# Kernel optimization log

Hardware: AMD Instinct MI355X
Metric: run time of the kernel (lower is better)

The kernel has to match this reference:

```python
import jax, jax.numpy as jnp
import numpy as np

N = 4096
D = 512
H = 3


def setup_inputs() -> dict:
    key = jax.random.key(0)
    k1, k2, k3 = jax.random.split(key, 3)
    graph_info = (jax.random.uniform(k1, (N, N)) < 0.01).astype(jnp.float32)
    h = jax.random.normal(k2, (N, D), dtype=jnp.float32)
    # xavier_normal_ with relu gain: std = sqrt(2) * sqrt(2/(fan_in+fan_out))
    std = np.sqrt(2.0) * np.sqrt(2.0 / (D + H))
    P = jax.random.normal(k3, (D, H), dtype=jnp.float32) * jnp.float32(std)
    return {"graph_info": graph_info, "h": h, "P": P}


def reference(graph_info, h, P):
    # graph_info_1 = spmm(graph_info^T, I)^T == graph_info (identity densification)
    mask = graph_info > 0                                  # [N, N]
    E = jax.nn.relu(h @ P)                                 # [N, H] per-node scores, all heads
    NEG = jnp.float32(-9e15)
    # e is broadcast along rows: att[i, j] = E[j, k] where edge (i->j) exists
    logits = jnp.where(mask[None, :, :], E.T[:, None, :], NEG)  # [H, N, N]
    att = jax.nn.softmax(logits, axis=-1)                  # row-softmax per head
    hh = jnp.einsum('hij,jd->hid', att, h)                 # [H, N, D] aggregate
    # sum_flag == 1: scale each row i by its degree (rowsum of graph_info_1)
    rowsum = jnp.sum(graph_info, axis=-1)                  # [N]
    hh = hh * rowsum[None, :, None]
    # multi_head > 1, concat=False: sum over heads
    return jnp.sum(hh, axis=0)                             # [N, D]
```

## Files before the change

### kernel.cpp

```cpp
#include <hip/hip_runtime.h>
#include <stdint.h>

#define NN 4096
#define DD 512
#define NH 3
#define MAXDEG 256

__device__ __forceinline__ unsigned short f2bf_rn(float x) {
    union { float f; uint32_t u; } v; v.f = x;
    uint32_t u = v.u;
    uint32_t r = (u + 0x7FFFu + ((u >> 16) & 1u)) >> 16;
    return (unsigned short)r;
}
__device__ __forceinline__ float bflo(uint32_t u) {
    union { uint32_t u; float f; } v; v.u = u << 16; return v.f;
}
__device__ __forceinline__ float bfhi(uint32_t u) {
    union { uint32_t u; float f; } v; v.u = u & 0xFFFF0000u; return v.f;
}

__global__ __launch_bounds__(256) void prep_kernel(
    const float* __restrict__ h, const float* __restrict__ P,
    float* __restrict__ w, unsigned short* __restrict__ hb)
{
    int gid = blockIdx.x * 256 + threadIdx.x;
    int row = gid >> 6, ln = gid & 63;
    const float4* h4 = (const float4*)(h + (size_t)row * DD);
    float4 va = h4[ln * 2], vb = h4[ln * 2 + 1];
    float e[8] = { va.x, va.y, va.z, va.w, vb.x, vb.y, vb.z, vb.w };

    uint32_t pk0 = (uint32_t)f2bf_rn(e[0]) | ((uint32_t)f2bf_rn(e[1]) << 16);
    uint32_t pk1 = (uint32_t)f2bf_rn(e[2]) | ((uint32_t)f2bf_rn(e[3]) << 16);
    uint32_t pk2 = (uint32_t)f2bf_rn(e[4]) | ((uint32_t)f2bf_rn(e[5]) << 16);
    uint32_t pk3 = (uint32_t)f2bf_rn(e[6]) | ((uint32_t)f2bf_rn(e[7]) << 16);
    uint4 pk = make_uint4(pk0, pk1, pk2, pk3);
    *(uint4*)(hb + (size_t)row * DD + ln * 8) = pk;

    int d0 = ln * 8;
    float a0 = 0.f, a1 = 0.f, a2 = 0.f;
    #pragma unroll
    for (int k = 0; k < 8; ++k) {
        float hv = e[k];
        const float* Pr = P + (size_t)(d0 + k) * NH;
        a0 = fmaf(hv, Pr[0], a0);
        a1 = fmaf(hv, Pr[1], a1);
        a2 = fmaf(hv, Pr[2], a2);
    }
    #pragma unroll
    for (int off = 32; off > 0; off >>= 1) {
        a0 += __shfl_down(a0, off);
        a1 += __shfl_down(a1, off);
        a2 += __shfl_down(a2, off);
    }
    if (ln == 0) {
        w[row * NH + 0] = expf(fmaxf(a0, 0.f));
        w[row * NH + 1] = expf(fmaxf(a1, 0.f));
        w[row * NH + 2] = expf(fmaxf(a2, 0.f));
    }
}

__global__ __launch_bounds__(256) void att_agg_kernel(
    const float* __restrict__ g, const unsigned short* __restrict__ hb,
    const float* __restrict__ w, float* __restrict__ out)
{
    __shared__ int   s_idx[MAXDEG + 4];
    __shared__ float s_c[MAXDEG + 4];
    __shared__ int   s_cnt;
    __shared__ float s_z[4][3];
    __shared__ float s_part[4][DD];

    const int row = blockIdx.x, tid = threadIdx.x;
    const int wv = tid >> 6, ln = tid & 63;
    if (tid == 0) s_cnt = 0;
    __syncthreads();

    const float4* g4 = (const float4*)(g + (size_t)row * NN);
    #pragma unroll
    for (int it = 0; it < (NN / 4) / 256; ++it) {
        int c4 = it * 256 + tid;
        float4 v = g4[c4];
        float comp[4] = { v.x, v.y, v.z, v.w };
        int base = c4 * 4;
        #pragma unroll
        for (int k = 0; k < 4; ++k) {
            bool p = comp[k] > 0.f;
            unsigned long long m = __ballot(p);
            if (m) {
                int nset = __popcll(m);
                int bpos;
                if (ln == 0) bpos = atomicAdd(&s_cnt, nset);
                bpos = __shfl(bpos, 0);
                if (p) {
                    unsigned pre = __builtin_amdgcn_mbcnt_lo((unsigned)m, 0u);
                    pre = __builtin_amdgcn_mbcnt_hi((unsigned)(m >> 32), pre);
                    int pos = bpos + (int)pre;
                    if (pos < MAXDEG) s_idx[pos] = base + k;
                }
            }
        }
    }
    __syncthreads();
    int nnz = s_cnt; if (nnz > MAXDEG) nnz = MAXDEG;

    if (nnz == 0) {
        ((float2*)(out + (size_t)row * DD))[tid] = make_float2(0.f, 0.f);
        return;
    }

    float z0 = 0.f, z1 = 0.f, z2 = 0.f, w0 = 0.f, w1 = 0.f, w2 = 0.f;
    int myj = 0;
    if (tid < nnz) {
        myj = s_idx[tid];
        const float* wr = w + (size_t)myj * NH;
        w0 = wr[0]; w1 = wr[1]; w2 = wr[2];
        z0 = w0; z1 = w1; z2 = w2;
    }
    #pragma unroll
    for (int off = 32; off > 0; off >>= 1) {
        z0 += __shfl_down(z0, off);
        z1 += __shfl_down(z1, off);
        z2 += __shfl_down(z2, off);
    }
    if (ln == 0) { s_z[wv][0] = z0; s_z[wv][1] = z1; s_z[wv][2] = z2; }
    __syncthreads();
    float Z0 = s_z[0][0] + s_z[1][0] + s_z[2][0] + s_z[3][0];
    float Z1 = s_z[0][1] + s_z[1][1] + s_z[2][1] + s_z[3][1];
    float Z2 = s_z[0][2] + s_z[1][2] + s_z[2][2] + s_z[3][2];
    float RS = (float)nnz;
    float sc0 = RS / Z0, sc1 = RS / Z1, sc2 = RS / Z2;

    int npad = (nnz + 3) & ~3;
    if (tid < nnz) s_c[tid] = fmaf(sc0, w0, fmaf(sc1, w1, sc2 * w2));
    else if (tid < npad) { s_idx[tid] = 0; s_c[tid] = 0.f; }
    __syncthreads();

    int nq = npad >> 2;
    float acc0=0.f,acc1=0.f,acc2=0.f,acc3=0.f,acc4=0.f,acc5=0.f,acc6=0.f,acc7=0.f;
    const unsigned short* hcol = hb + ln * 8;
    int q = 0;
    for (; q + 1 < nq; q += 2) {
        int t0 = q * 4 + wv, t1 = t0 + 4;
        int ja = s_idx[t0]; float ca = s_c[t0];
        int jb = s_idx[t1]; float cb = s_c[t1];
        uint4 ra = *(const uint4*)(hcol + (size_t)ja * DD);
        uint4 rb = *(const uint4*)(hcol + (size_t)jb * DD);
        acc0 = fmaf(ca, bflo(ra.x), acc0); acc1 = fmaf(ca, bfhi(ra.x), acc1);
        acc2 = fmaf(ca, bflo(ra.y), acc2); acc3 = fmaf(ca, bfhi(ra.y), acc3);
        acc4 = fmaf(ca, bflo(ra.z), acc4); acc5 = fmaf(ca, bfhi(ra.z), acc5);
        acc6 = fmaf(ca, bflo(ra.w), acc6); acc7 = fmaf(ca, bfhi(ra.w), acc7);
        acc0 = fmaf(cb, bflo(rb.x), acc0); acc1 = fmaf(cb, bfhi(rb.x), acc1);
        acc2 = fmaf(cb, bflo(rb.y), acc2); acc3 = fmaf(cb, bfhi(rb.y), acc3);
        acc4 = fmaf(cb, bflo(rb.z), acc4); acc5 = fmaf(cb, bfhi(rb.z), acc5);
        acc6 = fmaf(cb, bflo(rb.w), acc6); acc7 = fmaf(cb, bfhi(rb.w), acc7);
    }
    if (q < nq) {
        int t0 = q * 4 + wv;
        int ja = s_idx[t0]; float ca = s_c[t0];
        uint4 ra = *(const uint4*)(hcol + (size_t)ja * DD);
        acc0 = fmaf(ca, bflo(ra.x), acc0); acc1 = fmaf(ca, bfhi(ra.x), acc1);
        acc2 = fmaf(ca, bflo(ra.y), acc2); acc3 = fmaf(ca, bfhi(ra.y), acc3);
        acc4 = fmaf(ca, bflo(ra.z), acc4); acc5 = fmaf(ca, bfhi(ra.z), acc5);
        acc6 = fmaf(ca, bflo(ra.w), acc6); acc7 = fmaf(ca, bfhi(ra.w), acc7);
    }

    float4* sp = (float4*)&s_part[wv][ln * 8];
    sp[0] = make_float4(acc0, acc1, acc2, acc3);
    sp[1] = make_float4(acc4, acc5, acc6, acc7);
    __syncthreads();
    int c0 = tid * 2;
    float2 p0 = *(const float2*)&s_part[0][c0];
    float2 p1 = *(const float2*)&s_part[1][c0];
    float2 p2 = *(const float2*)&s_part[2][c0];
    float2 p3 = *(const float2*)&s_part[3][c0];
    float r0 = (p0.x + p1.x) + (p2.x + p3.x);
    float r1 = (p0.y + p1.y) + (p2.y + p3.y);
    ((float2*)(out + (size_t)row * DD))[tid] = make_float2(r0, r1);
}

extern "C" void kernel_launch(void* const* d_in, const int* in_sizes, int n_in,
                              void* d_out, int out_size, void* d_ws, size_t ws_size,
                              hipStream_t stream) {
    const float* g = (const float*)d_in[0];
    const float* h = (const float*)d_in[1];
    const float* P = (const float*)d_in[2];
    float* out = (float*)d_out;

    float* w = (float*)d_ws;
    unsigned short* hb = (unsigned short*)((char*)d_ws + 65536);

    prep_kernel<<<(NN * 64) / 256, 256, 0, stream>>>(h, P, w, hb);
    att_agg_kernel<<<NN, 256, 0, stream>>>(g, hb, w, out);
}
```

Before: 113.1 us.

## Process one row per wavefront and drop block-level synchronization

Each wavefront now handles a whole row: it scans the adjacency row, compacts neighbor indices into its own shared buffer, computes the softmax normalizers and gathers bf16 features alone. This removes shared atomics, __syncthreads and the cross-wave partial-sum reduction through shared memory, and launches a quarter as many blocks. Nontemporal loads and stores are used for the streamed adjacency, h and output. The trade-off is fewer waves per row, so each wave does a longer serial gather over all neighbors with less latency hiding per row.

```diff
diff --git a/kernel.cpp b/kernel.cpp
--- a/kernel.cpp
+++ b/kernel.cpp
@@ -5,6 +5,8 @@
 #define DD 512
 #define NH 3
 #define MAXDEG 256
+
+typedef float f4v __attribute__((ext_vector_type(4)));
 
 __device__ __forceinline__ unsigned short f2bf_rn(float x) {
     union { float f; uint32_t u; } v; v.f = x;
@@ -25,9 +27,10 @@
 {
     int gid = blockIdx.x * 256 + threadIdx.x;
     int row = gid >> 6, ln = gid & 63;
-    const float4* h4 = (const float4*)(h + (size_t)row * DD);
-    float4 va = h4[ln * 2], vb = h4[ln * 2 + 1];
-    float e[8] = { va.x, va.y, va.z, va.w, vb.x, vb.y, vb.z, vb.w };
+    const f4v* h4 = (const f4v*)(h + (size_t)row * DD);
+    f4v va = __builtin_nontemporal_load(&h4[ln * 2]);
+    f4v vb = __builtin_nontemporal_load(&h4[ln * 2 + 1]);
+    float e[8] = { va[0], va[1], va[2], va[3], vb[0], vb[1], vb[2], vb[3] };
 
     uint32_t pk0 = (uint32_t)f2bf_rn(e[0]) | ((uint32_t)f2bf_rn(e[1]) << 16);
     uint32_t pk1 = (uint32_t)f2bf_rn(e[2]) | ((uint32_t)f2bf_rn(e[3]) << 16);
@@ -63,118 +66,108 @@
     const float* __restrict__ g, const unsigned short* __restrict__ hb,
     const float* __restrict__ w, float* __restrict__ out)
 {
-    __shared__ int   s_idx[MAXDEG + 4];
-    __shared__ float s_c[MAXDEG + 4];
-    __shared__ int   s_cnt;
-    __shared__ float s_z[4][3];
-    __shared__ float s_part[4][DD];
+    __shared__ int   s_idx[4][MAXDEG + 8];
+    __shared__ float s_c[4][MAXDEG + 8];
 
-    const int row = blockIdx.x, tid = threadIdx.x;
-    const int wv = tid >> 6, ln = tid & 63;
-    if (tid == 0) s_cnt = 0;
-    __syncthreads();
+    const int wv = threadIdx.x >> 6, ln = threadIdx.x & 63;
+    const int row = blockIdx.x * 4 + wv;
+    int*   __restrict__ idxb = s_idx[wv];
+    float* __restrict__ cb   = s_c[wv];
 
-    const float4* g4 = (const float4*)(g + (size_t)row * NN);
-    #pragma unroll
-    for (int it = 0; it < (NN / 4) / 256; ++it) {
-        int c4 = it * 256 + tid;
-        float4 v = g4[c4];
-        float comp[4] = { v.x, v.y, v.z, v.w };
-        int base = c4 * 4;
+    const f4v* g4 = (const f4v*)(g + (size_t)row * NN);
+    int cnt = 0;
+    #pragma unroll 4
+    for (int it = 0; it < (NN / 4) / 64; ++it) {
+        f4v v = __builtin_nontemporal_load(&g4[it * 64 + ln]);
+        int base = (it * 64 + ln) * 4;
         #pragma unroll
         for (int k = 0; k < 4; ++k) {
-            bool p = comp[k] > 0.f;
+            bool p = v[k] > 0.f;
             unsigned long long m = __ballot(p);
             if (m) {
-                int nset = __popcll(m);
-                int bpos;
-                if (ln == 0) bpos = atomicAdd(&s_cnt, nset);
-                bpos = __shfl(bpos, 0);
                 if (p) {
                     unsigned pre = __builtin_amdgcn_mbcnt_lo((unsigned)m, 0u);
                     pre = __builtin_amdgcn_mbcnt_hi((unsigned)(m >> 32), pre);
-                    int pos = bpos + (int)pre;
-                    if (pos < MAXDEG) s_idx[pos] = base + k;
+                    int pos = cnt + (int)pre;
+                    if (pos < MAXDEG) idxb[pos] = base + k;
                 }
+                cnt += __popcll(m);
             }
         }
     }
-    __syncthreads();
-    int nnz = s_cnt; if (nnz > MAXDEG) nnz = MAXDEG;
+    int nnz = cnt > MAXDEG ? MAXDEG : cnt;
 
+    float* orow = out + (size_t)row * DD + ln * 8;
     if (nnz == 0) {
-        ((float2*)(out + (size_t)row * DD))[tid] = make_float2(0.f, 0.f);
+        f4v z = {0.f, 0.f, 0.f, 0.f};
+        __builtin_nontemporal_store(z, (f4v*)orow);
+        __builtin_nontemporal_store(z, (f4v*)(orow + 4));
         return;
     }
 
-    float z0 = 0.f, z1 = 0.f, z2 = 0.f, w0 = 0.f, w1 = 0.f, w2 = 0.f;
-    int myj = 0;
-    if (tid < nnz) {
-        myj = s_idx[tid];
-        const float* wr = w + (size_t)myj * NH;
-        w0 = wr[0]; w1 = wr[1]; w2 = wr[2];
-        z0 = w0; z1 = w1; z2 = w2;
+    __builtin_amdgcn_wave_barrier();
+
+    float z0 = 0.f, z1 = 0.f, z2 = 0.f;
+    for (int t = ln; t < nnz; t += 64) {
+        int j = idxb[t];
+        const float* wr = w + (size_t)j * NH;
+        z0 += wr[0]; z1 += wr[1]; z2 += wr[2];
     }
     #pragma unroll
     for (int off = 32; off > 0; off >>= 1) {
-        z0 += __shfl_down(z0, off);
-        z1 += __shfl_down(z1, off);
-        z2 += __shfl_down(z2, off);
+        z0 += __shfl_xor(z0, off);
+        z1 += __shfl_xor(z1, off);
+        z2 += __shfl_xor(z2, off);
     }
-    if (ln == 0) { s_z[wv][0] = z0; s_z[wv][1] = z1; s_z[wv][2] = z2; }
-    __syncthreads();
-    float Z0 = s_z[0][0] + s_z[1][0] + s_z[2][0] + s_z[3][0];
-    float Z1 = s_z[0][1] + s_z[1][1] + s_z[2][1] + s_z[3][1];
-    float Z2 = s_z[0][2] + s_z[1][2] + s_z[2][2] + s_z[3][2];
     float RS = (float)nnz;
-    float sc0 = RS / Z0, sc1 = RS / Z1, sc2 = RS / Z2;
+    float sc0 = RS / z0, sc1 = RS / z1, sc2 = RS / z2;
 
     int npad = (nnz + 3) & ~3;
-    if (tid < nnz) s_c[tid] = fmaf(sc0, w0, fmaf(sc1, w1, sc2 * w2));
-    else if (tid < npad) { s_idx[tid] = 0; s_c[tid] = 0.f; }
-    __syncthreads();
+    for (int t = ln; t < npad; t += 64) {
+        if (t < nnz) {
+            int j = idxb[t];
+            const float* wr = w + (size_t)j * NH;
+            cb[t] = fmaf(sc0, wr[0], fmaf(sc1, wr[1], sc2 * wr[2]));
+        } else {
+            idxb[t] = idxb[0];
+            cb[t] = 0.f;
+        }
+    }
+    __builtin_amdgcn_wave_barrier();
 
-    int nq = npad >> 2;
+    const unsigned short* hcol = hb + ln * 8;
     float acc0=0.f,acc1=0.f,acc2=0.f,acc3=0.f,acc4=0.f,acc5=0.f,acc6=0.f,acc7=0.f;
-    const unsigned short* hcol = hb + ln * 8;
-    int q = 0;
-    for (; q + 1 < nq; q += 2) {
-        int t0 = q * 4 + wv, t1 = t0 + 4;
-        int ja = s_idx[t0]; float ca = s_c[t0];
-        int jb = s_idx[t1]; float cb = s_c[t1];
-        uint4 ra = *(const uint4*)(hcol + (size_t)ja * DD);
-        uint4 rb = *(const uint4*)(hcol + (size_t)jb * DD);
-        acc0 = fmaf(ca, bflo(ra.x), acc0); acc1 = fmaf(ca, bfhi(ra.x), acc1);
-        acc2 = fmaf(ca, bflo(ra.y), acc2); acc3 = fmaf(ca, bfhi(ra.y), acc3);
-        acc4 = fmaf(ca, bflo(ra.z), acc4); acc5 = fmaf(ca, bfhi(ra.z), acc5);
-        acc6 = fmaf(ca, bflo(ra.w), acc6); acc7 = fmaf(ca, bfhi(ra.w), acc7);
-        acc0 = fmaf(cb, bflo(rb.x), acc0); acc1 = fmaf(cb, bfhi(rb.x), acc1);
-        acc2 = fmaf(cb, bflo(rb.y), acc2); acc3 = fmaf(cb, bfhi(rb.y), acc3);
-        acc4 = fmaf(cb, bflo(rb.z), acc4); acc5 = fmaf(cb, bfhi(rb.z), acc5);
-        acc6 = fmaf(cb, bflo(rb.w), acc6); acc7 = fmaf(cb, bfhi(rb.w), acc7);
-    }
-    if (q < nq) {
-        int t0 = q * 4 + wv;
-        int ja = s_idx[t0]; float ca = s_c[t0];
-        uint4 ra = *(const uint4*)(hcol + (size_t)ja * DD);
-        acc0 = fmaf(ca, bflo(ra.x), acc0); acc1 = fmaf(ca, bfhi(ra.x), acc1);
-        acc2 = fmaf(ca, bflo(ra.y), acc2); acc3 = fmaf(ca, bfhi(ra.y), acc3);
-        acc4 = fmaf(ca, bflo(ra.z), acc4); acc5 = fmaf(ca, bfhi(ra.z), acc5);
-        acc6 = fmaf(ca, bflo(ra.w), acc6); acc7 = fmaf(ca, bfhi(ra.w), acc7);
+    for (int t = 0; t < npad; t += 4) {
+        int j0 = idxb[t+0]; float c0 = cb[t+0];
+        int j1 = idxb[t+1]; float c1 = cb[t+1];
+        int j2 = idxb[t+2]; float c2 = cb[t+2];
+        int j3 = idxb[t+3]; float c3 = cb[t+3];
+        uint4 r0 = *(const uint4*)(hcol + (size_t)j0 * DD);
+        uint4 r1 = *(const uint4*)(hcol + (size_t)j1 * DD);
+        uint4 r2 = *(const uint4*)(hcol + (size_t)j2 * DD);
+        uint4 r3 = *(const uint4*)(hcol + (size_t)j3 * DD);
+        acc0 = fmaf(c0, bflo(r0.x), acc0); acc1 = fmaf(c0, bfhi(r0.x), acc1);
+        acc2 = fmaf(c0, bflo(r0.y), acc2); acc3 = fmaf(c0, bfhi(r0.y), acc3);
+        acc4 = fmaf(c0, bflo(r0.z), acc4); acc5 = fmaf(c0, bfhi(r0.z), acc5);
+        acc6 = fmaf(c0, bflo(r0.w), acc6); acc7 = fmaf(c0, bfhi(r0.w), acc7);
+        acc0 = fmaf(c1, bflo(r1.x), acc0); acc1 = fmaf(c1, bfhi(r1.x), acc1);
+        acc2 = fmaf(c1, bflo(r1.y), acc2); acc3 = fmaf(c1, bfhi(r1.y), acc3);
+        acc4 = fmaf(c1, bflo(r1.z), acc4); acc5 = fmaf(c1, bfhi(r1.z), acc5);
+        acc6 = fmaf(c1, bflo(r1.w), acc6); acc7 = fmaf(c1, bfhi(r1.w), acc7);
+        acc0 = fmaf(c2, bflo(r2.x), acc0); acc1 = fmaf(c2, bfhi(r2.x), acc1);
+        acc2 = fmaf(c2, bflo(r2.y), acc2); acc3 = fmaf(c2, bfhi(r2.y), acc3);
+        acc4 = fmaf(c2, bflo(r2.z), acc4); acc5 = fmaf(c2, bfhi(r2.z), acc5);
+        acc6 = fmaf(c2, bflo(r2.w), acc6); acc7 = fmaf(c2, bfhi(r2.w), acc7);
+        acc0 = fmaf(c3, bflo(r3.x), acc0); acc1 = fmaf(c3, bfhi(r3.x), acc1);
+        acc2 = fmaf(c3, bflo(r3.y), acc2); acc3 = fmaf(c3, bfhi(r3.y), acc3);
+        acc4 = fmaf(c3, bflo(r3.z), acc4); acc5 = fmaf(c3, bfhi(r3.z), acc5);
+        acc6 = fmaf(c3, bflo(r3.w), acc6); acc7 = fmaf(c3, bfhi(r3.w), acc7);
     }
 
-    float4* sp = (float4*)&s_part[wv][ln * 8];
-    sp[0] = make_float4(acc0, acc1, acc2, acc3);
-    sp[1] = make_float4(acc4, acc5, acc6, acc7);
-    __syncthreads();
-    int c0 = tid * 2;
-    float2 p0 = *(const float2*)&s_part[0][c0];
-    float2 p1 = *(const float2*)&s_part[1][c0];
-    float2 p2 = *(const float2*)&s_part[2][c0];
-    float2 p3 = *(const float2*)&s_part[3][c0];
-    float r0 = (p0.x + p1.x) + (p2.x + p3.x);
-    float r1 = (p0.y + p1.y) + (p2.y + p3.y);
-    ((float2*)(out + (size_t)row * DD))[tid] = make_float2(r0, r1);
+    f4v o0 = {acc0, acc1, acc2, acc3};
+    f4v o1 = {acc4, acc5, acc6, acc7};
+    __builtin_nontemporal_store(o0, (f4v*)orow);
+    __builtin_nontemporal_store(o1, (f4v*)(orow + 4));
 }
 
 extern "C" void kernel_launch(void* const* d_in, const int* in_sizes, int n_in,
@@ -189,5 +182,5 @@
     unsigned short* hb = (unsigned short*)((char*)d_ws + 65536);
 
     prep_kernel<<<(NN * 64) / 256, 256, 0, stream>>>(h, P, w, hb);
-    att_agg_kernel<<<NN, 256, 0, stream>>>(g, hb, w, out);
+    att_agg_kernel<<<NN / 4, 256, 0, stream>>>(g, hb, w, out);
 }
```

Result: slower. 118.0 us (+4.3%).
